# Kernel optimization log

Hardware: AMD Instinct MI355X
Metric: run time of the kernel (lower is better)

Reference implementation:

```python
import jax, jax.numpy as jnp
import numpy as np

EPS = 1e-6
BASE_CURVATURE = 1.0


def _artanh(x):
    return jnp.arctanh(jnp.clip(x, -1.0 + 1e-5, 1.0 - 1e-5))


def _norm(x):
    return jnp.maximum(jnp.linalg.norm(x, axis=-1, keepdims=True), EPS)


def _logmap0(x, c):
    # Poincare-ball log map at origin
    sc = jnp.sqrt(c)
    n = _norm(x)
    return _artanh(sc * n) * x / (sc * n)


def _expmap0(v, c):
    # Poincare-ball exp map at origin
    sc = jnp.sqrt(c)
    n = _norm(v)
    return jnp.tanh(sc * n) * v / (sc * n)


def _mobius_add(x, y, c):
    x2 = jnp.sum(x * x, axis=-1, keepdims=True)
    y2 = jnp.sum(y * y, axis=-1, keepdims=True)
    xy = jnp.sum(x * y, axis=-1, keepdims=True)
    num = (1.0 + 2.0 * c * xy + c * y2) * x + (1.0 - c * x2) * y
    den = 1.0 + 2.0 * c * xy + (c * c) * x2 * y2
    return num / jnp.maximum(den, EPS)


def _mobius_scalar_mul(t, x, c):
    sc = jnp.sqrt(c)
    n = _norm(x)
    return jnp.tanh(t * _artanh(sc * n)) * x / (sc * n)


def setup_inputs() -> dict:
    key = jax.random.key(0)
    ks = jax.random.split(key, 8)
    B, D_in, D_out, K = 4096, 2048, 2048, 4
    scale_w = np.sqrt(2.0 / (D_in + D_out)) * 0.1
    return {
        "x": jax.random.normal(ks[0], (B, D_in), jnp.float32) * 0.05,
        "weight": jax.random.normal(ks[1], (D_out, D_in), jnp.float32) * scale_w,
        "bias": jax.random.normal(ks[2], (D_out,), jnp.float32) * 0.01,
        "curv_weight": jax.random.normal(ks[3], (1, D_in), jnp.float32) * 0.1,
        "curv_bias": jnp.zeros((1,), jnp.float32),
        "anchors": jax.random.normal(ks[4], (K, D_out), jnp.float32) * 0.3,
        "t_values": jnp.full((K,), 0.5, jnp.float32),
        "anchor_weights": jnp.full((K,), 1.0 / K, jnp.float32),
    }


def reference(x, weight, bias, curv_weight, curv_bias, anchors, t_values, anchor_weights):
    # 1) dynamic curvature prediction: c_i = base_c * softplus(x . w + b), then mean
    logits = x @ curv_weight[0] + curv_bias[0]                 # [B]
    curvatures = BASE_CURVATURE * jax.nn.softplus(logits)      # [B]
    c = jax.lax.stop_gradient(jnp.mean(curvatures))            # scalar (.item() in torch)

    # 2) fused hyperbolic linear: expmap0(logmap0(x) @ W^T + b)
    u = _logmap0(x, c)                                         # [B, D_in]
    h = u @ weight.T + bias                                    # [B, D_out]
    y = _expmap0(h, c)                                         # [B, D_out]

    # 3) geodesic activation: weighted Mobius geodesic toward each anchor
    xe = y[:, None, :]                                         # [B, 1, D]
    a = anchors[None, :, :]                                    # [1, K, D]
    diff = _mobius_add(-xe, a, c)                              # [B, K, D]
    step = _mobius_scalar_mul(t_values[None, :, None], diff, c)
    g = _mobius_add(xe, step, c)                               # [B, K, D]
    w = jax.nn.softmax(anchor_weights)                         # [K]
    return jnp.einsum("bkd,k->bd", g, w)                       # [B, D_out]
```

## Files before the change

### kernel.cpp

```cpp
#include <hip/hip_runtime.h>
#include <stdint.h>

#define B_ROWS 4096
#define D_IN   2048
#define D_OUT  2048
#define KANCH  4

typedef _Float16 half8  __attribute__((ext_vector_type(8)));
typedef _Float16 half4  __attribute__((ext_vector_type(4)));
typedef float    floatx4 __attribute__((ext_vector_type(4)));
typedef const __attribute__((address_space(1))) uint8_t* gptr_t;
typedef __attribute__((address_space(3))) uint8_t* lptr_t;

__device__ __forceinline__ float frcp(float x)   { return __builtin_amdgcn_rcpf(x); }
__device__ __forceinline__ float ftanh(float x)  { float e = __expf(2.f * x); return (e - 1.f) * frcp(e + 1.f); }
__device__ __forceinline__ float fatanh(float z) { return 0.5f * __logf((1.f + z) * frcp(1.f - z)); }

__global__ __launch_bounds__(256) void k_prep(
    const float* __restrict__ x,
    const float* __restrict__ W,
    const float* __restrict__ cw,
    const float* __restrict__ cb,
    const float* __restrict__ bias,
    const float* __restrict__ anchors,
    _Float16* __restrict__ xh,
    _Float16* __restrict__ Wh,
    float* __restrict__ n2x,
    float* __restrict__ spart,
    float* __restrict__ scal)
{
    int tid = threadIdx.x;
    if (blockIdx.x < 1024) {
        int w = tid >> 6, lane = tid & 63;
        int row = blockIdx.x * 4 + w;
        const floatx4* xr = (const floatx4*)(x + (size_t)row * D_IN);
        const floatx4* wr = (const floatx4*)cw;
        _Float16* xo = xh + (size_t)row * D_IN;
        float dot = 0.f, ss = 0.f;
#pragma unroll
        for (int i = 0; i < 8; ++i) {
            int idx = i * 64 + lane;
            floatx4 xv = xr[idx];
            floatx4 wv = wr[idx];
#pragma unroll
            for (int j = 0; j < 4; ++j) {
                dot += xv[j] * wv[j];
                ss  += xv[j] * xv[j];
            }
            half4 h = {(_Float16)xv[0], (_Float16)xv[1], (_Float16)xv[2], (_Float16)xv[3]};
            *(half4*)(xo + idx * 4) = h;
        }
#pragma unroll
        for (int off = 32; off; off >>= 1) {
            dot += __shfl_down(dot, off);
            ss  += __shfl_down(ss, off);
        }
        __shared__ float spw[4];
        if (lane == 0) {
            n2x[row] = ss;
            float z = dot + cb[0];
            spw[w] = (z > 20.f) ? z : log1pf(expf(z));
        }
        __syncthreads();
        if (tid == 0)
            spart[blockIdx.x] = spw[0] + spw[1] + spw[2] + spw[3];
    } else if (blockIdx.x < 2048) {
        int blk = blockIdx.x - 1024;
        const floatx4* W4 = (const floatx4*)W;
#pragma unroll
        for (int i = 0; i < 4; ++i) {
            int idx = blk * 1024 + i * 256 + tid;
            floatx4 v = W4[idx];
            half4 h = {(_Float16)v[0], (_Float16)v[1], (_Float16)v[2], (_Float16)v[3]};
            *(half4*)(Wh + (size_t)idx * 4) = h;
        }
    } else {
        int w = tid >> 6, lane = tid & 63;
        float bf[8], af[KANCH][8];
        *(floatx4*)(bf)     = *(const floatx4*)(bias + tid * 8);
        *(floatx4*)(bf + 4) = *(const floatx4*)(bias + tid * 8 + 4);
#pragma unroll
        for (int k = 0; k < KANCH; ++k) {
            *(floatx4*)(af[k])     = *(const floatx4*)(anchors + (size_t)k * D_OUT + tid * 8);
            *(floatx4*)(af[k] + 4) = *(const floatx4*)(anchors + (size_t)k * D_OUT + tid * 8 + 4);
        }
        float v[9];
#pragma unroll
        for (int q = 0; q < 9; ++q) v[q] = 0.f;
#pragma unroll
        for (int j = 0; j < 8; ++j) {
            v[0] += bf[j] * bf[j];
#pragma unroll
            for (int k = 0; k < KANCH; ++k) {
                v[1 + k] += bf[j] * af[k][j];
                v[5 + k] += af[k][j] * af[k][j];
            }
        }
#pragma unroll
        for (int off = 32; off; off >>= 1)
#pragma unroll
            for (int q = 0; q < 9; ++q) v[q] += __shfl_down(v[q], off);
        __shared__ float red[4][9];
        if (lane == 0)
#pragma unroll
            for (int q = 0; q < 9; ++q) red[w][q] = v[q];
        __syncthreads();
        if (tid == 0)
#pragma unroll
            for (int q = 0; q < 9; ++q)
                scal[1 + q] = red[0][q] + red[1][q] + red[2][q] + red[3][q];
    }
}

template<int KPB>
__global__ __launch_bounds__(512, 4) void k_gemm(
    const _Float16* __restrict__ A,
    const _Float16* __restrict__ W,
    _Float16* __restrict__ P0,
    _Float16* __restrict__ P1)
{
    constexpr int NT = KPB / 32;
    constexpr int NZ = (KPB == D_IN) ? 1 : 2;
    __shared__ __align__(16) _Float16 lds[2][12288];
    const int tid  = threadIdx.x;
    const int lane = tid & 63;
    const int w    = tid >> 6;
    const int wm   = w >> 1;
    const int wn   = w & 1;

    int lin = (blockIdx.z * gridDim.y + blockIdx.y) * gridDim.x + blockIdx.x;
    int xcd = lin & 7;
    int i   = lin >> 3;
    int zz, mt, nt;
    if (NZ == 2) {
        zz = xcd & 1;
        int grp = xcd >> 1;
        mt = (grp >> 1) * 8 + (i >> 3);
        nt = (grp & 1) * 8 + (i & 7);
    } else {
        zz = 0;
        mt = (xcd >> 1) * 4 + (i >> 3);
        nt = (xcd & 1) * 8 + (i & 7);
    }
    const int bm0 = mt * 256;
    const int bn0 = nt * 128;
    const int kbase = zz * KPB;
    _Float16* P = (zz == 0) ? P0 : P1;

    const int srow = w * 16 + (lane & 15);
    const int scol = (lane >> 4) * 8;
    const size_t asrc = (size_t)(bm0 + srow) * D_IN + scol + kbase;
    const size_t bsrc = (size_t)(bn0 + srow) * D_IN + scol + kbase;
    const int eA = tid * 16;
    const int eB = 16384 + tid * 16;
    const int rA = wm * 4096 + lane * 16;
    const int rB = 16384 + wn * 4096 + lane * 16;

#define STAGE_T(Q, T) do { \
    uint8_t* qb_ = (uint8_t*)&lds[Q][0]; \
    size_t ko_ = (size_t)(T) * 32; \
    __builtin_amdgcn_global_load_lds((gptr_t)(A + asrc + ko_), (lptr_t)(qb_ + eA), 16, 0, 0); \
    __builtin_amdgcn_global_load_lds((gptr_t)(A + asrc + (size_t)128 * D_IN + ko_), (lptr_t)(qb_ + eA + 8192), 16, 0, 0); \
    __builtin_amdgcn_global_load_lds((gptr_t)(W + bsrc + ko_), (lptr_t)(qb_ + eB), 16, 0, 0); \
} while (0)

    floatx4 acc[4][4];
#pragma unroll
    for (int mi = 0; mi < 4; ++mi)
#pragma unroll
        for (int ni = 0; ni < 4; ++ni)
            acc[mi][ni] = (floatx4){0.f, 0.f, 0.f, 0.f};

    STAGE_T(0, 0);
    __syncthreads();

#define TILE_BODY(T, Q) do { \
    if ((T) + 1 < NT) STAGE_T((Q) ^ 1, (T) + 1); \
    half8 aq[4], bq[4]; \
    const uint8_t* qb_ = (const uint8_t*)&lds[Q][0]; \
    _Pragma("unroll") for (int mi = 0; mi < 4; ++mi) \
        aq[mi] = *(const half8*)(qb_ + rA + mi * 1024); \
    _Pragma("unroll") for (int ni = 0; ni < 4; ++ni) \
        bq[ni] = *(const half8*)(qb_ + rB + ni * 1024); \
    _Pragma("unroll") for (int mi = 0; mi < 4; ++mi) \
    _Pragma("unroll") for (int ni = 0; ni < 4; ++ni) \
        acc[mi][ni] = __builtin_amdgcn_mfma_f32_16x16x32_f16(aq[mi], bq[ni], acc[mi][ni], 0, 0, 0); \
    __syncthreads(); \
} while (0)

    for (int t = 0; t < NT; t += 2) {
        TILE_BODY(t, 0);
        TILE_BODY(t + 1, 1);
    }

#undef TILE_BODY
#undef STAGE_T

#pragma unroll
    for (int mi = 0; mi < 4; ++mi) {
#pragma unroll
        for (int r = 0; r < 4; ++r) {
            int gm = bm0 + wm * 64 + mi * 16 + (lane >> 4) * 4 + r;
#pragma unroll
            for (int ni = 0; ni < 4; ++ni) {
                int gn = bn0 + wn * 64 + ni * 16 + (lane & 15);
                P[(size_t)gm * D_OUT + gn] = (_Float16)acc[mi][ni][r];
            }
        }
    }
}

__global__ __launch_bounds__(256) void k_mobius(
    const _Float16* __restrict__ P0,
    const _Float16* __restrict__ P1,
    const float* __restrict__ bias,
    const float* __restrict__ anchors,
    const float* __restrict__ tv,
    const float* __restrict__ aw,
    const float* __restrict__ n2x,
    const float* __restrict__ spart,
    const float* __restrict__ scal,
    int split,
    float* __restrict__ out)
{
    int tid = threadIdx.x, w = tid >> 6, lane = tid & 63;
    size_t rowoff = (size_t)blockIdx.x * D_OUT;
    float pf[8], bf[8];
    {
        half8 p = *(const half8*)(P0 + rowoff + tid * 8);
#pragma unroll
        for (int j = 0; j < 8; ++j) pf[j] = (float)p[j];
    }
    if (split == 2) {
        half8 q = *(const half8*)(P1 + rowoff + tid * 8);
#pragma unroll
        for (int j = 0; j < 8; ++j) pf[j] += (float)q[j];
    }
    *(floatx4*)(bf)     = *(const floatx4*)(bias + tid * 8);
    *(floatx4*)(bf + 4) = *(const floatx4*)(bias + tid * 8 + 4);
    float af[KANCH][8];
#pragma unroll
    for (int k = 0; k < KANCH; ++k) {
        *(floatx4*)(af[k])     = *(const floatx4*)(anchors + (size_t)k * D_OUT + tid * 8);
        *(floatx4*)(af[k] + 4) = *(const floatx4*)(anchors + (size_t)k * D_OUT + tid * 8 + 4);
    }
    float v[7];
#pragma unroll
    for (int q = 0; q < 7; ++q) v[q] = 0.f;
    {
        floatx4 s4 = ((const floatx4*)spart)[tid];
        v[6] = s4[0] + s4[1] + s4[2] + s4[3];
    }
#pragma unroll
    for (int j = 0; j < 8; ++j) {
        v[0] += pf[j] * pf[j];
        v[1] += pf[j] * bf[j];
#pragma unroll
        for (int k = 0; k < KANCH; ++k) v[2 + k] += pf[j] * af[k][j];
    }
#pragma unroll
    for (int off = 32; off; off >>= 1)
#pragma unroll
        for (int q = 0; q < 7; ++q) v[q] += __shfl_down(v[q], off);
    __shared__ float red[4][7];
    __shared__ float cf[2 + KANCH];
    if (lane == 0)
#pragma unroll
        for (int q = 0; q < 7; ++q) red[w][q] = v[q];
    __syncthreads();
    if (w == 0) {
        int k = lane & 3;
        float pp = red[0][0] + red[1][0] + red[2][0] + red[3][0];
        float pb = red[0][1] + red[1][1] + red[2][1] + red[3][1];
        float pa = red[0][2 + k] + red[1][2 + k] + red[2][2 + k] + red[3][2 + k];
        float spsum = red[0][6] + red[1][6] + red[2][6] + red[3][6];
        float bb = scal[1];
        float ba = scal[2 + k];
        float aa = scal[6 + k];
        float c = spsum * (1.0f / (float)B_ROWS);
        float sc = __builtin_amdgcn_sqrtf(c);
        float nx = fmaxf(__builtin_amdgcn_sqrtf(n2x[blockIdx.x]), 1e-6f);
        float ax = sc * nx;
        float zx = fminf(fmaxf(ax, -1.f + 1e-5f), 1.f - 1e-5f);
        float f = fatanh(zx) * frcp(ax);
        float hh = f * f * pp + 2.f * f * pb + bb;
        float ha = f * pa + ba;
        float ek = __expf(aw[k]);
        float se = ek;
        se += __shfl_xor(se, 1);
        se += __shfl_xor(se, 2);
        float wk = ek * frcp(se);
        float nh = fmaxf(__builtin_amdgcn_sqrtf(hh), 1e-6f);
        float snh = sc * nh;
        float gy = ftanh(snh) * frcp(snh);
        float x2 = gy * gy * hh;
        float B1 = 1.f - c * x2;
        float y2 = aa;
        float dy = gy * ha;
        float A1 = 1.f - 2.f * c * dy + c * y2;
        float den1 = fmaxf(1.f - 2.f * c * dy + c * c * x2 * y2, 1e-6f);
        float rd1 = frcp(den1);
        float al = -A1 * rd1, be = B1 * rd1;
        float nd2 = fmaxf(al * al * x2 + 2.f * al * be * dy + be * be * y2, 0.f);
        float nd = fmaxf(__builtin_amdgcn_sqrtf(nd2), 1e-6f);
        float snd = sc * nd;
        float zc = fminf(fmaxf(snd, -1.f + 1e-5f), 1.f - 1e-5f);
        float s = ftanh(tv[k] * fatanh(zc)) * frcp(snd);
        float y2s = s * s * nd2;
        float xys = s * (al * x2 + be * dy);
        float A2 = 1.f + 2.f * c * xys + c * y2s;
        float den2 = fmaxf(1.f + 2.f * c * xys + c * c * x2 * y2s, 1e-6f);
        float rd2 = frcp(den2);
        float Cy  = (A2 + B1 * s * al) * rd2;
        float Cak = (B1 * s * be) * rd2;
        float chk = wk * Cy;
        chk += __shfl_xor(chk, 1);
        chk += __shfl_xor(chk, 2);
        if (lane == 0) {
            float c0 = gy * chk;
            cf[0] = c0 * f;
            cf[1] = c0;
        }
        if (lane < 4) cf[2 + lane] = wk * Cak;
    }
    __syncthreads();
    float cp = cf[0], cb_ = cf[1];
    float o[8];
#pragma unroll
    for (int j = 0; j < 8; ++j) {
        float val = cp * pf[j] + cb_ * bf[j];
#pragma unroll
        for (int k = 0; k < KANCH; ++k) val += cf[2 + k] * af[k][j];
        o[j] = val;
    }
    *(floatx4*)(out + rowoff + tid * 8)     = *(floatx4*)(o);
    *(floatx4*)(out + rowoff + tid * 8 + 4) = *(floatx4*)(o + 4);
}

extern "C" void kernel_launch(void* const* d_in, const int* in_sizes, int n_in,
                              void* d_out, int out_size, void* d_ws, size_t ws_size,
                              hipStream_t stream) {
    const float* x       = (const float*)d_in[0];
    const float* wt      = (const float*)d_in[1];
    const float* bias    = (const float*)d_in[2];
    const float* cw      = (const float*)d_in[3];
    const float* cb      = (const float*)d_in[4];
    const float* anchors = (const float*)d_in[5];
    const float* tv      = (const float*)d_in[6];
    const float* aw      = (const float*)d_in[7];
    float* out = (float*)d_out;

    _Float16* Wh = (_Float16*)d_ws;
    _Float16* xh = Wh + (size_t)D_OUT * D_IN;
    float* n2x   = (float*)(xh + (size_t)B_ROWS * D_IN);
    float* spart = n2x + B_ROWS;
    float* scal  = spart + 1024;
    _Float16* P0 = (_Float16*)(scal + 16);
    _Float16* P1 = P0 + (size_t)B_ROWS * D_OUT;
    size_t need2 = (size_t)((char*)(P1 + (size_t)B_ROWS * D_OUT) - (char*)d_ws);
    int split = (ws_size >= need2) ? 2 : 1;

    k_prep<<<2049, 256, 0, stream>>>(x, wt, cw, cb, bias, anchors, xh, Wh, n2x, spart, scal);
    if (split == 2)
        k_gemm<D_IN / 2><<<dim3(16, 16, 2), 512, 0, stream>>>(xh, Wh, P0, P1);
    else
        k_gemm<D_IN><<<dim3(16, 16, 1), 512, 0, stream>>>(xh, Wh, P0, P1);
    k_mobius<<<B_ROWS, 256, 0, stream>>>(P0, P1, bias, anchors, tv, aw, n2x, spart, scal, split, out);
}
```

Measured before the change: 171.1 us.

## Drop split-K GEMM, use triple-buffered K=64 pipeline with vmcnt waits

New measurement: 168.9 us. About the same (-1.3%).

```diff
diff --git a/kernel.cpp b/kernel.cpp
--- a/kernel.cpp
+++ b/kernel.cpp
@@ -33,22 +33,24 @@
     if (blockIdx.x < 1024) {
         int w = tid >> 6, lane = tid & 63;
         int row = blockIdx.x * 4 + w;
-        const floatx4* xr = (const floatx4*)(x + (size_t)row * D_IN);
-        const floatx4* wr = (const floatx4*)cw;
+        const float* xr = x + (size_t)row * D_IN;
         _Float16* xo = xh + (size_t)row * D_IN;
         float dot = 0.f, ss = 0.f;
 #pragma unroll
-        for (int i = 0; i < 8; ++i) {
-            int idx = i * 64 + lane;
-            floatx4 xv = xr[idx];
-            floatx4 wv = wr[idx];
+        for (int i = 0; i < 4; ++i) {
+            int base = i * 512 + lane * 8;
+            floatx4 a = *(const floatx4*)(xr + base);
+            floatx4 b = *(const floatx4*)(xr + base + 4);
+            floatx4 wa = *(const floatx4*)(cw + base);
+            floatx4 wb = *(const floatx4*)(cw + base + 4);
 #pragma unroll
             for (int j = 0; j < 4; ++j) {
-                dot += xv[j] * wv[j];
-                ss  += xv[j] * xv[j];
+                dot += a[j] * wa[j] + b[j] * wb[j];
+                ss  += a[j] * a[j] + b[j] * b[j];
             }
-            half4 h = {(_Float16)xv[0], (_Float16)xv[1], (_Float16)xv[2], (_Float16)xv[3]};
-            *(half4*)(xo + idx * 4) = h;
+            half8 h = {(_Float16)a[0], (_Float16)a[1], (_Float16)a[2], (_Float16)a[3],
+                       (_Float16)b[0], (_Float16)b[1], (_Float16)b[2], (_Float16)b[3]};
+            *(half8*)(xo + base) = h;
         }
 #pragma unroll
         for (int off = 32; off; off >>= 1) {
@@ -66,13 +68,16 @@
             spart[blockIdx.x] = spw[0] + spw[1] + spw[2] + spw[3];
     } else if (blockIdx.x < 2048) {
         int blk = blockIdx.x - 1024;
-        const floatx4* W4 = (const floatx4*)W;
-#pragma unroll
-        for (int i = 0; i < 4; ++i) {
-            int idx = blk * 1024 + i * 256 + tid;
-            floatx4 v = W4[idx];
-            half4 h = {(_Float16)v[0], (_Float16)v[1], (_Float16)v[2], (_Float16)v[3]};
-            *(half4*)(Wh + (size_t)idx * 4) = h;
+        const float* Wp = W + (size_t)blk * 4096;
+        _Float16* Wo = Wh + (size_t)blk * 4096;
+#pragma unroll
+        for (int i = 0; i < 2; ++i) {
+            int base = i * 2048 + tid * 8;
+            floatx4 a = *(const floatx4*)(Wp + base);
+            floatx4 b = *(const floatx4*)(Wp + base + 4);
+            half8 h = {(_Float16)a[0], (_Float16)a[1], (_Float16)a[2], (_Float16)a[3],
+                       (_Float16)b[0], (_Float16)b[1], (_Float16)b[2], (_Float16)b[3]};
+            *(half8*)(Wo + base) = h;
         }
     } else {
         int w = tid >> 6, lane = tid & 63;
@@ -112,56 +117,45 @@
     }
 }
 
-template<int KPB>
-__global__ __launch_bounds__(512, 4) void k_gemm(
+__global__ __launch_bounds__(512) void k_gemm(
     const _Float16* __restrict__ A,
     const _Float16* __restrict__ W,
-    _Float16* __restrict__ P0,
-    _Float16* __restrict__ P1)
+    _Float16* __restrict__ P)
 {
-    constexpr int NT = KPB / 32;
-    constexpr int NZ = (KPB == D_IN) ? 1 : 2;
-    __shared__ __align__(16) _Float16 lds[2][12288];
+    constexpr int NT = D_IN / 64;
+    __shared__ __align__(16) _Float16 lds[3][24576];
     const int tid  = threadIdx.x;
     const int lane = tid & 63;
     const int w    = tid >> 6;
     const int wm   = w >> 1;
     const int wn   = w & 1;
 
-    int lin = (blockIdx.z * gridDim.y + blockIdx.y) * gridDim.x + blockIdx.x;
+    int lin = blockIdx.y * gridDim.x + blockIdx.x;
     int xcd = lin & 7;
     int i   = lin >> 3;
-    int zz, mt, nt;
-    if (NZ == 2) {
-        zz = xcd & 1;
-        int grp = xcd >> 1;
-        mt = (grp >> 1) * 8 + (i >> 3);
-        nt = (grp & 1) * 8 + (i & 7);
-    } else {
-        zz = 0;
-        mt = (xcd >> 1) * 4 + (i >> 3);
-        nt = (xcd & 1) * 8 + (i & 7);
-    }
+    int mt  = (xcd >> 1) * 4 + (i >> 3);
+    int nt  = (xcd & 1) * 8 + (i & 7);
     const int bm0 = mt * 256;
     const int bn0 = nt * 128;
-    const int kbase = zz * KPB;
-    _Float16* P = (zz == 0) ? P0 : P1;
-
+
+    const int e0 = tid * 16;
     const int srow = w * 16 + (lane & 15);
     const int scol = (lane >> 4) * 8;
-    const size_t asrc = (size_t)(bm0 + srow) * D_IN + scol + kbase;
-    const size_t bsrc = (size_t)(bn0 + srow) * D_IN + scol + kbase;
-    const int eA = tid * 16;
-    const int eB = 16384 + tid * 16;
+    const size_t asrc = (size_t)(bm0 + srow) * D_IN + scol;
+    const size_t bsrc = (size_t)(bn0 + srow) * D_IN + scol;
     const int rA = wm * 4096 + lane * 16;
-    const int rB = 16384 + wn * 4096 + lane * 16;
-
-#define STAGE_T(Q, T) do { \
-    uint8_t* qb_ = (uint8_t*)&lds[Q][0]; \
-    size_t ko_ = (size_t)(T) * 32; \
-    __builtin_amdgcn_global_load_lds((gptr_t)(A + asrc + ko_), (lptr_t)(qb_ + eA), 16, 0, 0); \
-    __builtin_amdgcn_global_load_lds((gptr_t)(A + asrc + (size_t)128 * D_IN + ko_), (lptr_t)(qb_ + eA + 8192), 16, 0, 0); \
-    __builtin_amdgcn_global_load_lds((gptr_t)(W + bsrc + ko_), (lptr_t)(qb_ + eB), 16, 0, 0); \
+    const int rB = 32768 + wn * 4096 + lane * 16;
+
+#define GLL(SRC, DSTB) __builtin_amdgcn_global_load_lds((gptr_t)(SRC), (lptr_t)(DSTB), 16, 0, 0)
+#define STAGE6(BP, KT) do { \
+    uint8_t* b_ = (uint8_t*)(BP); \
+    size_t ko_ = (size_t)(KT) * 64; \
+    GLL(A + asrc + ko_,                        b_ + e0);                  \
+    GLL(A + asrc + (size_t)128 * D_IN + ko_,   b_ + 8192 + e0);           \
+    GLL(A + asrc + ko_ + 32,                   b_ + 16384 + e0);          \
+    GLL(A + asrc + (size_t)128 * D_IN + ko_ + 32, b_ + 24576 + e0);       \
+    GLL(W + bsrc + ko_,                        b_ + 32768 + e0);          \
+    GLL(W + bsrc + ko_ + 32,                   b_ + 40960 + e0);          \
 } while (0)
 
     floatx4 acc[4][4];
@@ -171,30 +165,50 @@
         for (int ni = 0; ni < 4; ++ni)
             acc[mi][ni] = (floatx4){0.f, 0.f, 0.f, 0.f};
 
-    STAGE_T(0, 0);
-    __syncthreads();
-
-#define TILE_BODY(T, Q) do { \
-    if ((T) + 1 < NT) STAGE_T((Q) ^ 1, (T) + 1); \
-    half8 aq[4], bq[4]; \
-    const uint8_t* qb_ = (const uint8_t*)&lds[Q][0]; \
+    uint8_t* base0 = (uint8_t*)&lds[0][0];
+    uint8_t* base1 = (uint8_t*)&lds[1][0];
+    uint8_t* base2 = (uint8_t*)&lds[2][0];
+
+    STAGE6(base0, 0);
+    STAGE6(base1, 1);
+
+    uint8_t *p0 = base0, *p1 = base1, *p2 = base2;
+
+#define TILE_READS_MFMA(BP) do { \
+    half8 aq0[4], bq0[4], aq1[4], bq1[4]; \
+    const uint8_t* b_ = (const uint8_t*)(BP); \
     _Pragma("unroll") for (int mi = 0; mi < 4; ++mi) \
-        aq[mi] = *(const half8*)(qb_ + rA + mi * 1024); \
+        aq0[mi] = *(const half8*)(b_ + rA + mi * 1024); \
     _Pragma("unroll") for (int ni = 0; ni < 4; ++ni) \
-        bq[ni] = *(const half8*)(qb_ + rB + ni * 1024); \
+        bq0[ni] = *(const half8*)(b_ + rB + ni * 1024); \
+    _Pragma("unroll") for (int mi = 0; mi < 4; ++mi) \
+        aq1[mi] = *(const half8*)(b_ + 16384 + rA + mi * 1024); \
+    _Pragma("unroll") for (int ni = 0; ni < 4; ++ni) \
+        bq1[ni] = *(const half8*)(b_ + 8192 + rB + ni * 1024); \
+    __builtin_amdgcn_s_setprio(1); \
     _Pragma("unroll") for (int mi = 0; mi < 4; ++mi) \
     _Pragma("unroll") for (int ni = 0; ni < 4; ++ni) \
-        acc[mi][ni] = __builtin_amdgcn_mfma_f32_16x16x32_f16(aq[mi], bq[ni], acc[mi][ni], 0, 0, 0); \
-    __syncthreads(); \
+        acc[mi][ni] = __builtin_amdgcn_mfma_f32_16x16x32_f16(aq0[mi], bq0[ni], acc[mi][ni], 0, 0, 0); \
+    _Pragma("unroll") for (int mi = 0; mi < 4; ++mi) \
+    _Pragma("unroll") for (int ni = 0; ni < 4; ++ni) \
+        acc[mi][ni] = __builtin_amdgcn_mfma_f32_16x16x32_f16(aq1[mi], bq1[ni], acc[mi][ni], 0, 0, 0); \
+    __builtin_amdgcn_s_setprio(0); \
 } while (0)
 
-    for (int t = 0; t < NT; t += 2) {
-        TILE_BODY(t, 0);
-        TILE_BODY(t + 1, 1);
-    }
-
-#undef TILE_BODY
-#undef STAGE_T
+    for (int T = 0; T < NT - 1; ++T) {
+        asm volatile("s_waitcnt vmcnt(6)" ::: "memory");
+        __builtin_amdgcn_s_barrier();
+        if (T + 2 < NT) STAGE6(p2, T + 2);
+        TILE_READS_MFMA(p0);
+        uint8_t* tmp = p0; p0 = p1; p1 = p2; p2 = tmp;
+    }
+    asm volatile("s_waitcnt vmcnt(0)" ::: "memory");
+    __builtin_amdgcn_s_barrier();
+    TILE_READS_MFMA(p0);
+
+#undef TILE_READS_MFMA
+#undef STAGE6
+#undef GLL
 
 #pragma unroll
     for (int mi = 0; mi < 4; ++mi) {
@@ -356,14 +370,8 @@
     float* spart = n2x + B_ROWS;
     float* scal  = spart + 1024;
     _Float16* P0 = (_Float16*)(scal + 16);
-    _Float16* P1 = P0 + (size_t)B_ROWS * D_OUT;
-    size_t need2 = (size_t)((char*)(P1 + (size_t)B_ROWS * D_OUT) - (char*)d_ws);
-    int split = (ws_size >= need2) ? 2 : 1;
 
     k_prep<<<2049, 256, 0, stream>>>(x, wt, cw, cb, bias, anchors, xh, Wh, n2x, spart, scal);
-    if (split == 2)
-        k_gemm<D_IN / 2><<<dim3(16, 16, 2), 512, 0, stream>>>(xh, Wh, P0, P1);
-    else
-        k_gemm<D_IN><<<dim3(16, 16, 1), 512, 0, stream>>>(xh, Wh, P0, P1);
-    k_mobius<<<B_ROWS, 256, 0, stream>>>(P0, P1, bias, anchors, tv, aw, n2x, spart, scal, split, out);
+    k_gemm<<<dim3(16, 16), 512, 0, stream>>>(xh, Wh, P0);
+    k_mobius<<<B_ROWS, 256, 0, stream>>>(P0, P0, bias, anchors, tv, aw, n2x, spart, scal, 1, out);
 }
```
